# Optimization experiments

Measured on AMD Instinct MI355X. Metric: run time of the kernel, lower is better.

Reference implementation:

```python
import jax, jax.numpy as jnp
import numpy as np

N = 8192
F_IN = 256
F_OUT = 128
SLOPE = 0.2
NEG_INF = -9000000000000000.0


def setup_inputs() -> dict:
    key = jax.random.key(0)
    k1, k2, k3, k4, k5 = jax.random.split(key, 5)
    x = jax.random.normal(k1, (N, F_IN), dtype=jnp.float32)
    adj = jax.random.randint(k2, (N, N), 0, 2).astype(jnp.float32)
    W = jax.random.normal(k3, (F_IN, F_OUT), dtype=jnp.float32) * (1.0 / np.sqrt(F_IN))
    a_src = jax.random.normal(k4, (F_OUT,), dtype=jnp.float32) * (1.0 / np.sqrt(F_OUT))
    a_dst = jax.random.normal(k5, (F_OUT,), dtype=jnp.float32) * (1.0 / np.sqrt(F_OUT))
    return {"x": x, "adj": adj, "W": W, "a_src": a_src, "a_dst": a_dst}


def reference(x, adj, W, a_src, a_dst):
    # h: (N, F_OUT)
    h = x @ W
    f_src = h @ a_src  # (N,)
    f_dst = h @ a_dst  # (N,)
    # additive attention scores: (N, N)
    e = f_src[:, None] + f_dst[None, :]
    e = jnp.where(e >= 0, e, SLOPE * e)  # leaky_relu
    e = jnp.where(adj > 0, e, NEG_INF)
    alpha = jax.nn.softmax(e, axis=1)  # (N, N)
    return alpha @ h  # (N, F_OUT)
```

## Files before the change

kernel.cpp:

```cpp
#include <hip/hip_runtime.h>
#include <hip/hip_bf16.h>

#define NN 8192
#define FIN 256
#define FO 128
#define ROWS 32
#define NCH 32
#define L2E 1.4426950408889634f
#define C2  0.28853900817779268f

typedef __bf16 bf16x8 __attribute__((ext_vector_type(8)));
typedef __bf16 bf16x2 __attribute__((ext_vector_type(2)));
typedef float  f32x4  __attribute__((ext_vector_type(4)));
typedef unsigned long long u64;
typedef u64 u64x2 __attribute__((ext_vector_type(2)));

__device__ __forceinline__ f32x4 ntload(const float* p) {
  return __builtin_nontemporal_load((const f32x4*)p);
}

__global__ __launch_bounds__(256) void k_proj(
    const float* __restrict__ x, const float* __restrict__ W,
    const float* __restrict__ a_src, const float* __restrict__ a_dst,
    __bf16* __restrict__ Bp, float* __restrict__ f_src, float* __restrict__ f_dst)
{
  __shared__ float xs[16 * FIN];
  __shared__ float fs[16], fd[16];
  const int tid = threadIdx.x;
  const int i0 = blockIdx.x * 16;

  const float4* xg = (const float4*)(x + (size_t)i0 * FIN);
  float4* xs4 = (float4*)xs;
  #pragma unroll
  for (int t = 0; t < 4; t++) xs4[tid + 256 * t] = xg[tid + 256 * t];
  if (tid < 16) { fs[tid] = 0.f; fd[tid] = 0.f; }
  __syncthreads();

  const int cq = tid & 31;
  const int rg = tid >> 5;
  const int c0 = cq * 4;
  const int r0 = rg * 2;
  float acc0[4] = {0.f,0.f,0.f,0.f};
  float acc1[4] = {0.f,0.f,0.f,0.f};
  const float* xr0 = xs + r0 * FIN;
  const float* xr1 = xs + (r0 + 1) * FIN;

  for (int k = 0; k < FIN; k += 4) {
    float4 xa = *(const float4*)(xr0 + k);
    float4 xb = *(const float4*)(xr1 + k);
    #pragma unroll
    for (int kk = 0; kk < 4; kk++) {
      float4 wv = *(const float4*)(W + (size_t)(k + kk) * FO + c0);
      float xav = ((const float*)&xa)[kk];
      float xbv = ((const float*)&xb)[kk];
      acc0[0] += xav * wv.x; acc0[1] += xav * wv.y;
      acc0[2] += xav * wv.z; acc0[3] += xav * wv.w;
      acc1[0] += xbv * wv.x; acc1[1] += xbv * wv.y;
      acc1[2] += xbv * wv.z; acc1[3] += xbv * wv.w;
    }
  }

  float4 as = *(const float4*)(a_src + c0);
  float4 ad = *(const float4*)(a_dst + c0);
  float ps0 = acc0[0]*as.x + acc0[1]*as.y + acc0[2]*as.z + acc0[3]*as.w;
  float ps1 = acc1[0]*as.x + acc1[1]*as.y + acc1[2]*as.z + acc1[3]*as.w;
  float pd0 = acc0[0]*ad.x + acc0[1]*ad.y + acc0[2]*ad.z + acc0[3]*ad.w;
  float pd1 = acc1[0]*ad.x + acc1[1]*ad.y + acc1[2]*ad.z + acc1[3]*ad.w;
  atomicAdd(&fs[r0],     ps0);
  atomicAdd(&fs[r0 + 1], ps1);
  atomicAdd(&fd[r0],     pd0);
  atomicAdd(&fd[r0 + 1], pd1);

  const int j0 = i0 + r0;
  const int kg = j0 >> 5;
  const int q  = (j0 >> 3) & 3;
  const int t0 = j0 & 7;
  #pragma unroll
  for (int c = 0; c < 4; c++) {
    const int n = c0 + c;
    bf16x2 v;
    v[0] = (__bf16)acc0[c];
    v[1] = (__bf16)acc1[c];
    size_t idx = ((size_t)(kg * 8 + (n >> 4)) * 64 + q * 16 + (n & 15)) * 8 + t0;
    *(bf16x2*)(Bp + idx) = v;
  }
  __syncthreads();
  if (tid < 16) { f_src[i0 + tid] = fs[tid]; f_dst[i0 + tid] = fd[tid]; }
}

__global__ __launch_bounds__(640) void k_attn(
    const float* __restrict__ adj, const __bf16* __restrict__ Bp,
    const float* __restrict__ f_src, const float* __restrict__ f_dst,
    float* __restrict__ out)
{
  __shared__ __align__(16) float G1[NN];
  __shared__ __align__(16) float G2[NN];
  __shared__ __align__(16) u64 msk[2][ROWS][5];
  __shared__ float lsum[ROWS];

  const int tid = threadIdx.x;
  const int w = tid >> 6;
  const int lane = tid & 63;
  const int i0 = blockIdx.x * ROWS;

  if (w >= 8) {
    const int pw = w - 8;
    const int prow0 = pw * 16;
    const float* abase = adj + (size_t)(i0 + prow0) * NN + lane * 4;

    f32x4 s0,s1,s2,s3,s4,s5,s6,s7,s8,s9,s10,s11,s12,s13,s14,s15;

#define PLOAD(c) {                                                            \
    const float* _b = abase + (size_t)(c) * 256;                              \
    s0=ntload(_b);        s1=ntload(_b+NN);       s2=ntload(_b+2*NN);         \
    s3=ntload(_b+3*NN);   s4=ntload(_b+4*NN);     s5=ntload(_b+5*NN);         \
    s6=ntload(_b+6*NN);   s7=ntload(_b+7*NN);     s8=ntload(_b+8*NN);         \
    s9=ntload(_b+9*NN);   s10=ntload(_b+10*NN);   s11=ntload(_b+11*NN);       \
    s12=ntload(_b+12*NN); s13=ntload(_b+13*NN);   s14=ntload(_b+14*NN);       \
    s15=ntload(_b+15*NN); }

#define PROW(sv, slot, r) {                                                   \
    u64 b0=__ballot(sv[0]>0.f), b1=__ballot(sv[1]>0.f);                       \
    u64 b2=__ballot(sv[2]>0.f), b3=__ballot(sv[3]>0.f);                       \
    if (lane < 4)                                                             \
      msk[slot][prow0 + (r)][lane] = lane==0?b0:lane==1?b1:lane==2?b2:b3; }

#define PPACK(slot) {                                                         \
    PROW(s0,slot,0)  PROW(s1,slot,1)  PROW(s2,slot,2)  PROW(s3,slot,3)        \
    PROW(s4,slot,4)  PROW(s5,slot,5)  PROW(s6,slot,6)  PROW(s7,slot,7)        \
    PROW(s8,slot,8)  PROW(s9,slot,9)  PROW(s10,slot,10) PROW(s11,slot,11)     \
    PROW(s12,slot,12) PROW(s13,slot,13) PROW(s14,slot,14) PROW(s15,slot,15) }

    PLOAD(0)
    PPACK(0)
    PLOAD(1)
    asm volatile("s_waitcnt lgkmcnt(0)" ::: "memory");
    __builtin_amdgcn_s_barrier();
    __builtin_amdgcn_sched_barrier(0);

    for (int k = 0; k < NCH; ++k) {
      if (k + 1 < NCH) {
        PPACK((k + 1) & 1)
        if (k + 2 < NCH) PLOAD(k + 2)
      }
      asm volatile("s_waitcnt lgkmcnt(0)" ::: "memory");
      __builtin_amdgcn_s_barrier();
      __builtin_amdgcn_sched_barrier(0);
    }
    __syncthreads();
#undef PLOAD
#undef PROW
#undef PPACK
  } else {
    const int m = lane & 15;
    const int q = lane >> 4;
    const int mt = w >> 2;
    const int nq = w & 3;

    const int ctid = tid;
    #pragma unroll
    for (int t = 0; t < NN / 512; ++t) {
      int j = t * 512 + ctid;
      float d = f_dst[j];
      G1[j] = __builtin_amdgcn_exp2f(d * L2E);
      G2[j] = __builtin_amdgcn_exp2f(d * C2);
    }
    float s = f_src[i0 + mt * 16 + m];
    const float F1 = __builtin_amdgcn_exp2f(s * L2E);
    const float F2 = __builtin_amdgcn_exp2f(s * C2);

    f32x4 acc0 = (f32x4){0.f, 0.f, 0.f, 0.f};
    f32x4 acc1 = (f32x4){0.f, 0.f, 0.f, 0.f};
    float psum = 0.f;
    const int r0l = mt * 16 + m;

    __syncthreads();

    for (int c = 0; c < NCH; ++c) {
      const int cur = c & 1;
      u64x2 Ma01 = *(const u64x2*)&msk[cur][r0l][0];
      u64x2 Ma23 = *(const u64x2*)&msk[cur][r0l][2];
      const u64 M0 = Ma01[0], M1 = Ma01[1], M2 = Ma23[0], M3 = Ma23[1];

      #pragma unroll
      for (int ss = 0; ss < 4; ++ss) {
        #pragma unroll
        for (int kg = 0; kg < 2; ++kg) {
          const int jj = c * 256 + ss * 64 + kg * 32 + q * 8;
          float4 u0 = *(const float4*)(G1 + jj);
          float4 u1 = *(const float4*)(G1 + jj + 4);
          float4 v0 = *(const float4*)(G2 + jj);
          float4 v1 = *(const float4*)(G2 + jj + 4);
          const unsigned b = ss * 16 + kg * 8 + q * 2;
          const unsigned e0 = (unsigned)(M0 >> b);
          const unsigned e1 = (unsigned)(M1 >> b);
          const unsigned e2 = (unsigned)(M2 >> b);
          const unsigned e3 = (unsigned)(M3 >> b);
          float p0 = (e0 & 1u) ? fmaxf(F1 * u0.x, F2 * v0.x) : 0.f;
          float p1 = (e1 & 1u) ? fmaxf(F1 * u0.y, F2 * v0.y) : 0.f;
          float p2 = (e2 & 1u) ? fmaxf(F1 * u0.z, F2 * v0.z) : 0.f;
          float p3 = (e3 & 1u) ? fmaxf(F1 * u0.w, F2 * v0.w) : 0.f;
          float p4 = (e0 & 2u) ? fmaxf(F1 * u1.x, F2 * v1.x) : 0.f;
          float p5 = (e1 & 2u) ? fmaxf(F1 * u1.y, F2 * v1.y) : 0.f;
          float p6 = (e2 & 2u) ? fmaxf(F1 * u1.z, F2 * v1.z) : 0.f;
          float p7 = (e3 & 2u) ? fmaxf(F1 * u1.w, F2 * v1.w) : 0.f;
          if (nq == 0)
            psum += ((p0 + p1) + (p2 + p3)) + ((p4 + p5) + (p6 + p7));
          bf16x8 a;
          a[0] = (__bf16)p0; a[1] = (__bf16)p1; a[2] = (__bf16)p2;
          a[3] = (__bf16)p3; a[4] = (__bf16)p4; a[5] = (__bf16)p5;
          a[6] = (__bf16)p6; a[7] = (__bf16)p7;

          const __bf16* bsrc = Bp + (size_t)(c * 8 + ss * 2 + kg) * 4096
                               + (size_t)(nq * 2) * 512 + lane * 8;
          bf16x8 bf0 = *(const bf16x8*)bsrc;
          bf16x8 bf1 = *(const bf16x8*)(bsrc + 512);
          acc0 = __builtin_amdgcn_mfma_f32_16x16x32_bf16(a, bf0, acc0, 0, 0, 0);
          acc1 = __builtin_amdgcn_mfma_f32_16x16x32_bf16(a, bf1, acc1, 0, 0, 0);
        }
      }
      __syncthreads();
    }

    if (nq == 0) {
      float p = psum;
      p += __shfl_xor(p, 16);
      p += __shfl_xor(p, 32);
      if (lane < 16) lsum[mt * 16 + lane] = p;
    }
    __syncthreads();

    const int rr0 = mt * 16 + q * 4;
    #pragma unroll
    for (int r = 0; r < 4; ++r) {
      const float inv = 1.0f / lsum[rr0 + r];
      float* orow = out + (size_t)(i0 + rr0 + r) * FO + (nq * 2) * 16 + m;
      orow[0]  = acc0[r] * inv;
      orow[16] = acc1[r] * inv;
    }
  }
}

extern "C" void kernel_launch(void* const* d_in, const int* in_sizes, int n_in,
                              void* d_out, int out_size, void* d_ws, size_t ws_size,
                              hipStream_t stream) {
  const float* x     = (const float*)d_in[0];
  const float* adj   = (const float*)d_in[1];
  const float* W     = (const float*)d_in[2];
  const float* a_src = (const float*)d_in[3];
  const float* a_dst = (const float*)d_in[4];
  float* out = (float*)d_out;

  char* ws = (char*)d_ws;
  __bf16* Bp   = (__bf16*)ws;
  float* f_src = (float*)(ws + 2097152);
  float* f_dst = (float*)(ws + 2097152 + 32768);

  hipLaunchKernelGGL(k_proj, dim3(512), dim3(256), 0, stream,
                     x, W, a_src, a_dst, Bp, f_src, f_dst);
  hipLaunchKernelGGL(k_attn, dim3(256), dim3(640), 0, stream,
                     adj, Bp, f_src, f_dst, out);
}
```

Baseline: 448.8 us.

## Split attention-weight computation across waves and share via LDS

Previously each of the 4 column-quarter waves per row tile recomputed all 8 masked exp-weight fragments for a chunk. Now each wave computes only its own 64-column slice (2 fragments), writes the bf16 A fragments to a double-buffered LDS array, and after a barrier all waves read the 8 fragments back to run their MFMAs. Row sums are accumulated with LDS atomics instead of being computed by one wave. This cuts redundant VALU exp/select/convert work by 4x. In exchange it adds LDS traffic and a second barrier in the loop's critical path.

```diff
diff --git a/kernel.cpp b/kernel.cpp
--- a/kernel.cpp
+++ b/kernel.cpp
@@ -96,6 +96,7 @@
   __shared__ __align__(16) float G1[NN];
   __shared__ __align__(16) float G2[NN];
   __shared__ __align__(16) u64 msk[2][ROWS][5];
+  __shared__ __align__(16) __bf16 af[2][2][8][64][8];
   __shared__ float lsum[ROWS];
 
   const int tid = threadIdx.x;
@@ -155,16 +156,17 @@
     const int m = lane & 15;
     const int q = lane >> 4;
     const int mt = w >> 2;
+    const int ss = w & 3;
     const int nq = w & 3;
 
-    const int ctid = tid;
     #pragma unroll
     for (int t = 0; t < NN / 512; ++t) {
-      int j = t * 512 + ctid;
+      int j = t * 512 + tid;
       float d = f_dst[j];
       G1[j] = __builtin_amdgcn_exp2f(d * L2E);
       G2[j] = __builtin_amdgcn_exp2f(d * C2);
     }
+    if (tid < ROWS) lsum[tid] = 0.f;
     float s = f_src[i0 + mt * 16 + m];
     const float F1 = __builtin_amdgcn_exp2f(s * L2E);
     const float F2 = __builtin_amdgcn_exp2f(s * C2);
@@ -178,12 +180,11 @@
 
     for (int c = 0; c < NCH; ++c) {
       const int cur = c & 1;
-      u64x2 Ma01 = *(const u64x2*)&msk[cur][r0l][0];
-      u64x2 Ma23 = *(const u64x2*)&msk[cur][r0l][2];
-      const u64 M0 = Ma01[0], M1 = Ma01[1], M2 = Ma23[0], M3 = Ma23[1];
-
-      #pragma unroll
-      for (int ss = 0; ss < 4; ++ss) {
+
+      {
+        u64x2 Ma01 = *(const u64x2*)&msk[cur][r0l][0];
+        u64x2 Ma23 = *(const u64x2*)&msk[cur][r0l][2];
+        const u64 M0 = Ma01[0], M1 = Ma01[1], M2 = Ma23[0], M3 = Ma23[1];
         #pragma unroll
         for (int kg = 0; kg < 2; ++kg) {
           const int jj = c * 256 + ss * 64 + kg * 32 + q * 8;
@@ -204,29 +205,50 @@
           float p5 = (e1 & 2u) ? fmaxf(F1 * u1.y, F2 * v1.y) : 0.f;
           float p6 = (e2 & 2u) ? fmaxf(F1 * u1.z, F2 * v1.z) : 0.f;
           float p7 = (e3 & 2u) ? fmaxf(F1 * u1.w, F2 * v1.w) : 0.f;
-          if (nq == 0)
-            psum += ((p0 + p1) + (p2 + p3)) + ((p4 + p5) + (p6 + p7));
+          psum += ((p0 + p1) + (p2 + p3)) + ((p4 + p5) + (p6 + p7));
           bf16x8 a;
           a[0] = (__bf16)p0; a[1] = (__bf16)p1; a[2] = (__bf16)p2;
           a[3] = (__bf16)p3; a[4] = (__bf16)p4; a[5] = (__bf16)p5;
           a[6] = (__bf16)p6; a[7] = (__bf16)p7;
-
-          const __bf16* bsrc = Bp + (size_t)(c * 8 + ss * 2 + kg) * 4096
-                               + (size_t)(nq * 2) * 512 + lane * 8;
-          bf16x8 bf0 = *(const bf16x8*)bsrc;
-          bf16x8 bf1 = *(const bf16x8*)(bsrc + 512);
-          acc0 = __builtin_amdgcn_mfma_f32_16x16x32_bf16(a, bf0, acc0, 0, 0, 0);
-          acc1 = __builtin_amdgcn_mfma_f32_16x16x32_bf16(a, bf1, acc1, 0, 0, 0);
+          *(bf16x8*)&af[cur][mt][ss * 2 + kg][lane][0] = a;
         }
       }
       __syncthreads();
-    }
-
-    if (nq == 0) {
+
+      {
+        const __bf16* bch = Bp + (size_t)c * 8 * 4096 + (size_t)(nq * 2) * 512 + lane * 8;
+        const bf16x8* afp = (const bf16x8*)&af[cur][mt][0][lane][0];
+        #pragma unroll
+        for (int h = 0; h < 2; ++h) {
+          bf16x8 b00 = *(const bf16x8*)(bch + (h * 4 + 0) * 4096);
+          bf16x8 b10 = *(const bf16x8*)(bch + (h * 4 + 0) * 4096 + 512);
+          bf16x8 b01 = *(const bf16x8*)(bch + (h * 4 + 1) * 4096);
+          bf16x8 b11 = *(const bf16x8*)(bch + (h * 4 + 1) * 4096 + 512);
+          bf16x8 b02 = *(const bf16x8*)(bch + (h * 4 + 2) * 4096);
+          bf16x8 b12 = *(const bf16x8*)(bch + (h * 4 + 2) * 4096 + 512);
+          bf16x8 b03 = *(const bf16x8*)(bch + (h * 4 + 3) * 4096);
+          bf16x8 b13 = *(const bf16x8*)(bch + (h * 4 + 3) * 4096 + 512);
+          bf16x8 a0 = afp[(h * 4 + 0) * 64];
+          bf16x8 a1 = afp[(h * 4 + 1) * 64];
+          bf16x8 a2 = afp[(h * 4 + 2) * 64];
+          bf16x8 a3 = afp[(h * 4 + 3) * 64];
+          acc0 = __builtin_amdgcn_mfma_f32_16x16x32_bf16(a0, b00, acc0, 0, 0, 0);
+          acc1 = __builtin_amdgcn_mfma_f32_16x16x32_bf16(a0, b10, acc1, 0, 0, 0);
+          acc0 = __builtin_amdgcn_mfma_f32_16x16x32_bf16(a1, b01, acc0, 0, 0, 0);
+          acc1 = __builtin_amdgcn_mfma_f32_16x16x32_bf16(a1, b11, acc1, 0, 0, 0);
+          acc0 = __builtin_amdgcn_mfma_f32_16x16x32_bf16(a2, b02, acc0, 0, 0, 0);
+          acc1 = __builtin_amdgcn_mfma_f32_16x16x32_bf16(a2, b12, acc1, 0, 0, 0);
+          acc0 = __builtin_amdgcn_mfma_f32_16x16x32_bf16(a3, b03, acc0, 0, 0, 0);
+          acc1 = __builtin_amdgcn_mfma_f32_16x16x32_bf16(a3, b13, acc1, 0, 0, 0);
+        }
+      }
+    }
+
+    {
       float p = psum;
       p += __shfl_xor(p, 16);
       p += __shfl_xor(p, 32);
-      if (lane < 16) lsum[mt * 16 + lane] = p;
+      if (lane < 16) atomicAdd(&lsum[mt * 16 + lane], p);
     }
     __syncthreads();
 
```

New measurement: 402.9 us. 1.11x faster.
